# Kernel optimization log

Measured on AMD Instinct MI355X. Metric: run time of the kernel, lower is better.

The kernel has to match this reference:

```python
import jax, jax.numpy as jnp
import numpy as np

B, T, D_IN, H, C = 4096, 20, 300, 512, 10


def setup_inputs() -> dict:
    key = jax.random.key(0)
    ks = jax.random.split(key, 12)
    s = lambda fan_in, fan_out: float(np.sqrt(6.0 / (fan_in + fan_out)))  # xavier uniform bound
    u = lambda k, shape, b: jax.random.uniform(k, shape, jnp.float32, -b, b)
    return {
        "x": jax.random.normal(ks[0], (B, T, D_IN), jnp.float32),
        "W_emb": u(ks[1], (D_IN, H), s(D_IN, H)),
        "b_emb": jnp.zeros((H,), jnp.float32),
        "wx0": u(ks[2], (H, H), s(H, H)),
        "wh0": u(ks[3], (H, H), s(H, H)),
        "b0": jnp.zeros((H,), jnp.float32),
        "wx1": u(ks[4], (H, H), s(H, H)),
        "wh1": u(ks[5], (H, H), s(H, H)),
        "b1": jnp.zeros((H,), jnp.float32),
        "wx2": u(ks[6], (H, H), s(H, H)),
        "wh2": u(ks[7], (H, H), s(H, H)),
        "b2": jnp.zeros((H,), jnp.float32),
        "W_fc": u(ks[8], (H, C), s(H, C)),
        "b_fc": jnp.zeros((C,), jnp.float32),
    }


def reference(x, W_emb, b_emb, wx0, wh0, b0, wx1, wh1, b1, wx2, wh2, b2, W_fc, b_fc):
    # embedding_layer applied to all timesteps: [B,T,300] -> [B,T,512]
    emb = jnp.einsum("btd,dh->bth", x, W_emb) + b_emb
    h0 = jnp.zeros((x.shape[0], wx0.shape[1]), x.dtype)
    init = (h0, h0, h0)

    def step(carry, v_t):  # v_t: [B,H]
        h0, h1, h2 = carry
        h0 = jnp.tanh(v_t @ wx0 + h0 @ wh0 + b0)
        h1 = jnp.tanh(h0 @ wx1 + h1 @ wh1 + b1)
        h2 = jnp.tanh(h1 @ wx2 + h2 @ wh2 + b2)
        return (h0, h1, h2), None

    (h0, h1, h2), _ = jax.lax.scan(step, init, jnp.swapaxes(emb, 0, 1))  # scan over T
    return h2 @ W_fc + b_fc  # [B, C]
```

## Files before the change

kernel.cpp:

```cpp
#include <hip/hip_runtime.h>

typedef _Float16 f16;
typedef _Float16 f16x8 __attribute__((ext_vector_type(8)));
typedef float floatx4 __attribute__((ext_vector_type(4)));

__device__ __forceinline__ float ftanh(float x) {
  float ax = __builtin_fabsf(x);
  float e  = __expf(-2.0f * ax);
  float t  = (1.0f - e) * __builtin_amdgcn_rcpf(1.0f + e);
  return x < 0.0f ? -t : t;
}

__device__ __forceinline__ void gll16(const f16* g, f16* l) {
  __builtin_amdgcn_global_load_lds(
      (const __attribute__((address_space(1))) void*)g,
      (__attribute__((address_space(3))) void*)l, 16, 0, 0);
}

template<int FJ>
__device__ __forceinline__ void tile_gemm(
    const f16* __restrict__ A0, int ldA0,
    const f16* __restrict__ A1, int ldA1,
    int K, const f16* __restrict__ WT,
    const float* __restrict__ bias,
    f16* __restrict__ outp, int bm, int bn, f16* sm)
{
  const int tid  = threadIdx.x;
  const int w    = tid >> 6;
  const int lane = tid & 63;
  const int lm   = lane & 15;
  const int quad = lane >> 4;
  const int wm   = (w >> 1) * 64;
  const int wn   = (w & 1) * (FJ * 16);
  const int srow8 = lane >> 3;
  const int scol  = ((lane & 7) ^ srow8) * 8;
  const int lmx   = lane & 7;
  constexpr int SB = 8192 + FJ * 2048;

  floatx4 acc[4][FJ];
  #pragma unroll
  for (int i = 0; i < 4; ++i)
    #pragma unroll
    for (int j = 0; j < FJ; ++j)
      acc[i][j] = (floatx4){0.f, 0.f, 0.f, 0.f};

  auto stage = [&](int buf, int k0) {
    const f16* Asrc = (k0 < 512) ? (A0 + k0) : (A1 + (k0 - 512));
    const int  ld   = (k0 < 512) ? ldA0 : ldA1;
    f16* As0 = sm + buf * SB;
    f16* Ws0 = As0 + 8192;
    #pragma unroll
    for (int i = 0; i < 4; ++i) {
      int r = (w * 4 + i) * 8 + srow8;
      gll16(Asrc + (size_t)(bm + r) * ld + scol, As0 + (w * 4 + i) * 512);
    }
    #pragma unroll
    for (int i = 0; i < FJ; ++i) {
      int r = (w * FJ + i) * 8 + srow8;
      gll16(WT + (size_t)(bn + r) * K + k0 + scol, Ws0 + (w * FJ + i) * 512);
    }
  };

  const int NS = K >> 6;
  stage(0, 0);
  __syncthreads();
  for (int s = 0; s < NS; ++s) {
    if (s + 1 < NS) stage((s + 1) & 1, (s + 1) << 6);
    const f16* As0 = sm + (s & 1) * SB;
    const f16* Ws0 = As0 + 8192;
    #pragma unroll
    for (int kk = 0; kk < 64; kk += 32) {
      const int sw = (((kk >> 3) + quad) ^ lmx) << 3;
      f16x8 a[4], bfr[FJ];
      #pragma unroll
      for (int fi = 0; fi < 4; ++fi)
        a[fi] = *(const f16x8*)&As0[(size_t)(wm + fi * 16 + lm) * 64 + sw];
      #pragma unroll
      for (int fj = 0; fj < FJ; ++fj)
        bfr[fj] = *(const f16x8*)&Ws0[(size_t)(wn + fj * 16 + lm) * 64 + sw];
      #pragma unroll
      for (int fi = 0; fi < 4; ++fi)
        #pragma unroll
        for (int fj = 0; fj < FJ; ++fj)
          acc[fi][fj] = __builtin_amdgcn_mfma_f32_16x16x32_f16(a[fi], bfr[fj], acc[fi][fj], 0, 0, 0);
    }
    __syncthreads();
  }

  constexpr int ES = FJ * 32 + 8;
  #pragma unroll
  for (int fi = 0; fi < 4; ++fi)
    #pragma unroll
    for (int fj = 0; fj < FJ; ++fj) {
      int col = wn + fj * 16 + lm;
      #pragma unroll
      for (int r = 0; r < 4; ++r) {
        int row = wm + fi * 16 + quad * 4 + r;
        sm[row * ES + col] = (f16)acc[fi][fj][r];
      }
    }
  __syncthreads();
  constexpr int TPR = (FJ * 32) / 8;
  constexpr int RPP = 256 / TPR;
  #pragma unroll
  for (int p = 0; p < 128 / RPP; ++p) {
    int row = p * RPP + tid / TPR;
    int c8  = (tid % TPR) * 8;
    f16x8 ve = *(const f16x8*)&sm[row * ES + c8];
    floatx4 bv0 = *(const floatx4*)&bias[bn + c8];
    floatx4 bv1 = *(const floatx4*)&bias[bn + c8 + 4];
    union { f16 e[8]; f16x8 v; } o;
    #pragma unroll
    for (int j = 0; j < 4; ++j) o.e[j]     = (f16)ftanh((float)ve[j]     + bv0[j]);
    #pragma unroll
    for (int j = 0; j < 4; ++j) o.e[4 + j] = (f16)ftanh((float)ve[4 + j] + bv1[j]);
    *(f16x8*)(outp + (size_t)(bm + row) * 512 + bn + c8) = o.v;
  }
}

__global__ __launch_bounds__(256, 3)
void rnn_step(int wv, const f16* __restrict__ xh,
              const f16* __restrict__ W0T, const f16* __restrict__ W1T,
              const f16* __restrict__ W2T,
              const float* __restrict__ bcomb, const float* __restrict__ b1,
              const float* __restrict__ b2,
              const f16* __restrict__ H0c, f16* __restrict__ H0n,
              const f16* __restrict__ H1c, f16* __restrict__ H1n,
              const f16* __restrict__ H2c, f16* __restrict__ H2n)
{
  __shared__ f16 sm[24576];
  const int b   = blockIdx.x;
  const int xcd = b & 7;
  const int r   = b >> 3;
  const int slab = xcd * 4 + (r & 3);
  const int bn   = ((r >> 2) & 7) * 64;

  if (r < 32) {
    if (wv > 19) return;
    tile_gemm<2>(H0c, 512, xh + (size_t)wv * 320, 6400, 832, W0T, bcomb,
                 H0n, slab * 128, bn, sm);
  } else if (r < 64) {
    if (wv < 1 || wv > 20) return;
    tile_gemm<2>(H0c, 512, H1c, 512, 1024, W1T, b1, H1n, slab * 128, bn, sm);
  } else {
    if (wv < 2) return;
    tile_gemm<2>(H1c, 512, H2c, 512, 1024, W2T, b2, H2n, slab * 128, bn, sm);
  }
}

#define PX_N 1600

__global__ __launch_bounds__(256)
void prep_x(const float* __restrict__ x, f16* __restrict__ xh)
{
  const int NTH = PX_N * 256;
  const int g = blockIdx.x * 256 + threadIdx.x;
  floatx4 va[8], vb[8];
  int rw[8], cc[8];
  const floatx4 z4 = {0.f, 0.f, 0.f, 0.f};
  #pragma unroll
  for (int s = 0; s < 8; ++s) {
    int U = g + s * NTH;
    int row = U / 40;
    int c   = (U - row * 40) * 8;
    rw[s] = row; cc[s] = c;
    const float* src = x + (size_t)row * 300 + c;
    va[s] = (c + 4 <= 300) ? *(const floatx4*)src : z4;
    vb[s] = (c + 8 <= 300) ? *(const floatx4*)(src + 4) : z4;
  }
  #pragma unroll
  for (int s = 0; s < 8; ++s) {
    union { f16 e[8]; f16x8 v; } t;
    #pragma unroll
    for (int j = 0; j < 4; ++j) { t.e[j] = (f16)va[s][j]; t.e[4 + j] = (f16)vb[s][j]; }
    *(f16x8*)(xh + (size_t)rw[s] * 320 + cc[s]) = t.v;
  }
}

#define PW_WCE 2560
#define PW_BC  2568
#define PW_WT  3208
#define PW_Z   6280

__global__ __launch_bounds__(256)
void prep_w(const float* __restrict__ W_emb, const float* __restrict__ b_emb,
            const float* __restrict__ wx0, const float* __restrict__ wh0,
            const float* __restrict__ b0,
            const float* __restrict__ wx1, const float* __restrict__ wh1,
            const float* __restrict__ wx2, const float* __restrict__ wh2,
            f16* __restrict__ W0T, f16* __restrict__ W1T, f16* __restrict__ W2T,
            float* __restrict__ bcomb,
            f16* __restrict__ H0a, f16* __restrict__ H1b, f16* __restrict__ H2a)
{
  __shared__ float red[256];
  const int b   = blockIdx.x;
  const int tid = threadIdx.x;

  if (b < PW_WCE) {
    int oidx  = b * 64 + (tid & 63);
    int chunk = tid >> 6;
    int n = oidx & 511, k = oidx >> 9;
    float s = 0.f;
    if (k < 300) {
      const float* we = W_emb + k * 512 + chunk * 128;
      const float* wx = wx0 + (size_t)(chunk * 128) * 512 + n;
      #pragma unroll 4
      for (int j = 0; j < 128; ++j)
        s = __builtin_fmaf(we[j], wx[(size_t)j * 512], s);
    }
    red[tid] = s;
    __syncthreads();
    if (chunk == 0)
      W0T[(size_t)n * 832 + 512 + k] =
          (f16)(red[tid] + red[tid + 64] + red[tid + 128] + red[tid + 192]);
  } else if (b < PW_BC) {
    int n     = (b - PW_WCE) * 64 + (tid & 63);
    int chunk = tid >> 6;
    float s = 0.f;
    const float* be = b_emb + chunk * 128;
    const float* wx = wx0 + (size_t)(chunk * 128) * 512 + n;
    #pragma unroll 4
    for (int j = 0; j < 128; ++j)
      s = __builtin_fmaf(be[j], wx[(size_t)j * 512], s);
    red[tid] = s;
    __syncthreads();
    if (chunk == 0)
      bcomb[n] = b0[n] + red[tid] + red[tid + 64] + red[tid + 128] + red[tid + 192];
  } else if (b < PW_WT) {
    int id = (b - PW_BC) * 256 + tid;
    if (id < 32768) {
      int n = id & 511, k8 = id >> 9;
      union { f16 e[8]; f16x8 v; } t;
      #pragma unroll
      for (int j = 0; j < 8; ++j) t.e[j] = (f16)wh0[(size_t)(k8 * 8 + j) * 512 + n];
      *(f16x8*)&W0T[(size_t)n * 832 + k8 * 8] = t.v;
    } else if (id < 98304) {
      int i2 = id - 32768;
      int n = i2 & 511, k8 = i2 >> 9;
      union { f16 e[8]; f16x8 v; } t;
      const float* src = (k8 < 64) ? (wx1 + (size_t)(k8 * 8) * 512 + n)
                                   : (wh1 + (size_t)((k8 - 64) * 8) * 512 + n);
      #pragma unroll
      for (int j = 0; j < 8; ++j) t.e[j] = (f16)src[(size_t)j * 512];
      *(f16x8*)&W1T[(size_t)n * 1024 + k8 * 8] = t.v;
    } else {
      int i2 = id - 98304;
      int n = i2 & 511, k8 = i2 >> 9;
      union { f16 e[8]; f16x8 v; } t;
      const float* src = (k8 < 64) ? (wx2 + (size_t)(k8 * 8) * 512 + n)
                                   : (wh2 + (size_t)((k8 - 64) * 8) * 512 + n);
      #pragma unroll
      for (int j = 0; j < 8; ++j) t.e[j] = (f16)src[(size_t)j * 512];
      *(f16x8*)&W2T[(size_t)n * 1024 + k8 * 8] = t.v;
    }
  } else {
    int id = (b - PW_WT) * 256 + tid;
    f16x8 z8 = {};
    f16* dst = (id < 262144) ? H0a : (id < 524288) ? H1b : H2a;
    *(f16x8*)(dst + (size_t)(id & 262143) * 8) = z8;
  }
}

__global__ void fc_kernel(const f16* __restrict__ h2,
                          const float* __restrict__ Wfc, const float* __restrict__ bfc,
                          float* __restrict__ out)
{
  __shared__ float wf[5120];
  __shared__ float bf[16];
  const int tid = threadIdx.x;
  for (int i = tid; i < 5120; i += 256) wf[i] = Wfc[i];
  if (tid < 10) bf[tid] = bfc[tid];
  __syncthreads();
  int id = blockIdx.x * 256 + tid;
  int row = id / 10;
  int c = id - row * 10;
  float s = bf[c];
  const f16* hr = h2 + (size_t)row * 512;
  for (int k8 = 0; k8 < 64; ++k8) {
    f16x8 h8 = *(const f16x8*)(hr + k8 * 8);
    #pragma unroll
    for (int j = 0; j < 8; ++j)
      s = __builtin_fmaf((float)h8[j], wf[(k8 * 8 + j) * 10 + c], s);
  }
  out[id] = s;
}

extern "C" void kernel_launch(void* const* d_in, const int* in_sizes, int n_in,
                              void* d_out, int out_size, void* d_ws, size_t ws_size,
                              hipStream_t stream)
{
  (void)in_sizes; (void)n_in; (void)out_size; (void)ws_size;
  const float* x     = (const float*)d_in[0];
  const float* W_emb = (const float*)d_in[1];
  const float* b_emb = (const float*)d_in[2];
  const float* wx0   = (const float*)d_in[3];
  const float* wh0   = (const float*)d_in[4];
  const float* b0    = (const float*)d_in[5];
  const float* wx1   = (const float*)d_in[6];
  const float* wh1   = (const float*)d_in[7];
  const float* b1    = (const float*)d_in[8];
  const float* wx2   = (const float*)d_in[9];
  const float* wh2   = (const float*)d_in[10];
  const float* b2    = (const float*)d_in[11];
  const float* W_fc  = (const float*)d_in[12];
  const float* b_fc  = (const float*)d_in[13];
  float* out = (float*)d_out;

  char* ws = (char*)d_ws;
  size_t off = 0;
  auto alloc = [&](size_t bytes) -> void* {
    void* p = ws + off;
    off = (off + bytes + 255) & ~(size_t)255;
    return p;
  };
  f16*   xh    = (f16*)alloc((size_t)81920 * 320 * 2);
  f16*   W0T   = (f16*)alloc((size_t)512 * 832 * 2);
  f16*   W1T   = (f16*)alloc((size_t)512 * 1024 * 2);
  f16*   W2T   = (f16*)alloc((size_t)512 * 1024 * 2);
  float* bcomb = (float*)alloc(512 * 4);
  f16*   H0a   = (f16*)alloc((size_t)4096 * 512 * 2);
  f16*   H0b   = (f16*)alloc((size_t)4096 * 512 * 2);
  f16*   H1a   = (f16*)alloc((size_t)4096 * 512 * 2);
  f16*   H1b   = (f16*)alloc((size_t)4096 * 512 * 2);
  f16*   H2a   = (f16*)alloc((size_t)4096 * 512 * 2);
  f16*   H2b   = (f16*)alloc((size_t)4096 * 512 * 2);

  prep_x<<<PX_N, 256, 0, stream>>>(x, xh);
  prep_w<<<PW_Z, 256, 0, stream>>>(W_emb, b_emb, wx0, wh0, b0,
                                   wx1, wh1, wx2, wh2,
                                   W0T, W1T, W2T, bcomb, H0a, H1b, H2a);

  for (int wv = 0; wv < 22; ++wv) {
    const int cur = wv & 1;
    f16* H0c = cur ? H0b : H0a;  f16* H0n = cur ? H0a : H0b;
    f16* H1c = cur ? H1b : H1a;  f16* H1n = cur ? H1a : H1b;
    f16* H2c = cur ? H2b : H2a;  f16* H2n = cur ? H2a : H2b;
    rnn_step<<<768, 256, 0, stream>>>(wv, xh, W0T, W1T, W2T, bcomb, b1, b2,
                                      H0c, H0n, H1c, H1n, H2c, H2n);
  }

  fc_kernel<<<160, 256, 0, stream>>>(H2a, W_fc, b_fc, out);
}
```

Before: 626.6 us.

## Load weight fragments directly to registers and widen tiles for layers 1-2

```diff
diff --git a/kernel.cpp b/kernel.cpp
--- a/kernel.cpp
+++ b/kernel.cpp
@@ -17,11 +17,11 @@
       (__attribute__((address_space(3))) void*)l, 16, 0, 0);
 }
 
-template<int FJ>
+template<int FJ, int K>
 __device__ __forceinline__ void tile_gemm(
     const f16* __restrict__ A0, int ldA0,
     const f16* __restrict__ A1, int ldA1,
-    int K, const f16* __restrict__ WT,
+    const f16* __restrict__ WT,
     const float* __restrict__ bias,
     f16* __restrict__ outp, int bm, int bn, f16* sm)
 {
@@ -35,7 +35,8 @@
   const int srow8 = lane >> 3;
   const int scol  = ((lane & 7) ^ srow8) * 8;
   const int lmx   = lane & 7;
-  constexpr int SB = 8192 + FJ * 2048;
+  constexpr int SB = 8192;
+  constexpr int NS = K / 64;
 
   floatx4 acc[4][FJ];
   #pragma unroll
@@ -44,45 +45,53 @@
     for (int j = 0; j < FJ; ++j)
       acc[i][j] = (floatx4){0.f, 0.f, 0.f, 0.f};
 
-  auto stage = [&](int buf, int k0) {
-    const f16* Asrc = (k0 < 512) ? (A0 + k0) : (A1 + (k0 - 512));
-    const int  ld   = (k0 < 512) ? ldA0 : ldA1;
-    f16* As0 = sm + buf * SB;
-    f16* Ws0 = As0 + 8192;
-    #pragma unroll
-    for (int i = 0; i < 4; ++i) {
-      int r = (w * 4 + i) * 8 + srow8;
-      gll16(Asrc + (size_t)(bm + r) * ld + scol, As0 + (w * 4 + i) * 512);
-    }
-    #pragma unroll
-    for (int i = 0; i < FJ; ++i) {
-      int r = (w * FJ + i) * 8 + srow8;
-      gll16(WT + (size_t)(bn + r) * K + k0 + scol, Ws0 + (w * FJ + i) * 512);
-    }
-  };
-
-  const int NS = K >> 6;
-  stage(0, 0);
+  const f16* wp = WT + (size_t)(bn + wn + lm) * K + quad * 8;
+
+  f16x8 bfr[2][FJ][2];
+  #pragma unroll
+  for (int fj = 0; fj < FJ; ++fj) {
+    bfr[0][fj][0] = *(const f16x8*)(wp + (size_t)fj * 16 * K);
+    bfr[0][fj][1] = *(const f16x8*)(wp + (size_t)fj * 16 * K + 32);
+  }
+  #pragma unroll
+  for (int i = 0; i < 4; ++i) {
+    int r = (w * 4 + i) * 8 + srow8;
+    gll16(A0 + (size_t)(bm + r) * ldA0 + scol, sm + (w * 4 + i) * 512);
+  }
   __syncthreads();
+
+  #pragma unroll
   for (int s = 0; s < NS; ++s) {
-    if (s + 1 < NS) stage((s + 1) & 1, (s + 1) << 6);
+    if (s + 1 < NS) {
+      const int k0n = (s + 1) * 64;
+      #pragma unroll
+      for (int fj = 0; fj < FJ; ++fj) {
+        bfr[(s + 1) & 1][fj][0] = *(const f16x8*)(wp + (size_t)fj * 16 * K + k0n);
+        bfr[(s + 1) & 1][fj][1] = *(const f16x8*)(wp + (size_t)fj * 16 * K + k0n + 32);
+      }
+      const f16* Asrc = (k0n < 512) ? (A0 + k0n) : (A1 + (k0n - 512));
+      const int  ld   = (k0n < 512) ? ldA0 : ldA1;
+      f16* As1 = sm + ((s + 1) & 1) * SB;
+      #pragma unroll
+      for (int i = 0; i < 4; ++i) {
+        int r = (w * 4 + i) * 8 + srow8;
+        gll16(Asrc + (size_t)(bm + r) * ld + scol, As1 + (w * 4 + i) * 512);
+      }
+    }
     const f16* As0 = sm + (s & 1) * SB;
-    const f16* Ws0 = As0 + 8192;
     #pragma unroll
     for (int kk = 0; kk < 64; kk += 32) {
       const int sw = (((kk >> 3) + quad) ^ lmx) << 3;
-      f16x8 a[4], bfr[FJ];
+      f16x8 a[4];
       #pragma unroll
       for (int fi = 0; fi < 4; ++fi)
         a[fi] = *(const f16x8*)&As0[(size_t)(wm + fi * 16 + lm) * 64 + sw];
-      #pragma unroll
-      for (int fj = 0; fj < FJ; ++fj)
-        bfr[fj] = *(const f16x8*)&Ws0[(size_t)(wn + fj * 16 + lm) * 64 + sw];
       #pragma unroll
       for (int fi = 0; fi < 4; ++fi)
         #pragma unroll
         for (int fj = 0; fj < FJ; ++fj)
-          acc[fi][fj] = __builtin_amdgcn_mfma_f32_16x16x32_f16(a[fi], bfr[fj], acc[fi][fj], 0, 0, 0);
+          acc[fi][fj] = __builtin_amdgcn_mfma_f32_16x16x32_f16(
+              a[fi], bfr[s & 1][fj][kk >> 5], acc[fi][fj], 0, 0, 0);
     }
     __syncthreads();
   }
@@ -118,7 +127,7 @@
   }
 }
 
-__global__ __launch_bounds__(256, 3)
+__global__ __launch_bounds__(256, 2)
 void rnn_step(int wv, const f16* __restrict__ xh,
               const f16* __restrict__ W0T, const f16* __restrict__ W1T,
               const f16* __restrict__ W2T,
@@ -128,23 +137,29 @@
               const f16* __restrict__ H1c, f16* __restrict__ H1n,
               const f16* __restrict__ H2c, f16* __restrict__ H2n)
 {
-  __shared__ f16 sm[24576];
+  __shared__ f16 sm[17408];
   const int b   = blockIdx.x;
   const int xcd = b & 7;
   const int r   = b >> 3;
-  const int slab = xcd * 4 + (r & 3);
-  const int bn   = ((r >> 2) & 7) * 64;
 
   if (r < 32) {
     if (wv > 19) return;
-    tile_gemm<2>(H0c, 512, xh + (size_t)wv * 320, 6400, 832, W0T, bcomb,
-                 H0n, slab * 128, bn, sm);
-  } else if (r < 64) {
+    const int slab = xcd * 4 + (r & 3);
+    const int bn   = (r >> 2) * 64;
+    tile_gemm<2, 832>(H0c, 512, xh + (size_t)wv * 320, 6400, W0T, bcomb,
+                      H0n, slab * 128, bn, sm);
+  } else if (r < 48) {
     if (wv < 1 || wv > 20) return;
-    tile_gemm<2>(H0c, 512, H1c, 512, 1024, W1T, b1, H1n, slab * 128, bn, sm);
+    const int rr   = r - 32;
+    const int slab = xcd * 4 + (rr & 3);
+    const int bn   = (rr >> 2) * 128;
+    tile_gemm<4, 1024>(H0c, 512, H1c, 512, W1T, b1, H1n, slab * 128, bn, sm);
   } else {
     if (wv < 2) return;
-    tile_gemm<2>(H1c, 512, H2c, 512, 1024, W2T, b2, H2n, slab * 128, bn, sm);
+    const int rr   = r - 48;
+    const int slab = xcd * 4 + (rr & 3);
+    const int bn   = (rr >> 2) * 128;
+    tile_gemm<4, 1024>(H1c, 512, H2c, 512, W2T, b2, H2n, slab * 128, bn, sm);
   }
 }
 
@@ -335,7 +350,7 @@
     f16* H0c = cur ? H0b : H0a;  f16* H0n = cur ? H0a : H0b;
     f16* H1c = cur ? H1b : H1a;  f16* H1n = cur ? H1a : H1b;
     f16* H2c = cur ? H2b : H2a;  f16* H2n = cur ? H2a : H2b;
-    rnn_step<<<768, 256, 0, stream>>>(wv, xh, W0T, W1T, W2T, bcomb, b1, b2,
+    rnn_step<<<512, 256, 0, stream>>>(wv, xh, W0T, W1T, W2T, bcomb, b1, b2,
                                       H0c, H0n, H1c, H1n, H2c, H2n);
   }
 
```

Result: slower. 862.0 us (+37.6%).
